# Kernel optimization log

Hardware: AMD Instinct MI355X
Metric: run time of the kernel (lower is better)

## Reference

```python
import jax, jax.numpy as jnp
import numpy as np

L, C, H = 4, 512, 8
HD = C // H

def silu(x):
    return x * jax.nn.sigmoid(x)

def layernorm(x, g, b, eps=1e-5):
    m = x.mean(-1, keepdims=True)
    v = ((x - m) ** 2).mean(-1, keepdims=True)
    return (x - m) * jax.lax.rsqrt(v + eps) * g + b

def adaln(x, t, w, b):
    # x: (N,B,C), t: (B,C), w: (2C,C), b: (2C,)
    mod = silu(t) @ w.T + b
    scale, shift = jnp.split(mod, 2, axis=-1)
    return x * (1.0 + scale[None]) + shift[None]

def embed_rotary(x, pos):
    # x: (B,N,C), pos: (B,N,C,2) with [...,0]=cos, [...,1]=sin
    cos, sin = pos[..., 0], pos[..., 1]
    x2 = jnp.stack([-x[..., 1::2], x[..., 0::2]], axis=-1).reshape(x.shape)
    return x * cos + x2 * sin

def setup_inputs() -> dict:
    key = jax.random.key(0)
    ks = jax.random.split(key, 24)
    Nq, Nkv, B = 1024, 2048, 4
    query = jax.random.normal(ks[0], (Nq, B, C), jnp.float32)
    value = jax.random.normal(ks[1], (Nkv, B, C), jnp.float32)
    diff_ts = jax.random.normal(ks[2], (B, C), jnp.float32)
    # valid rotary codes: cos/sin of random angles
    aq = jax.random.uniform(ks[3], (B, Nq, C), jnp.float32, 0.0, 2 * np.pi)
    ak = jax.random.uniform(ks[4], (B, Nkv, C), jnp.float32, 0.0, 2 * np.pi)
    query_pos = jnp.stack([jnp.cos(aq), jnp.sin(aq)], axis=-1)
    value_pos = jnp.stack([jnp.cos(ak), jnp.sin(ak)], axis=-1)
    s = 0.02
    inp = dict(query=query, value=value, diff_ts=diff_ts,
               query_pos=query_pos, value_pos=value_pos,
               aw_attn=jax.random.normal(ks[5], (L, 2 * C, C)) * s,
               ab_attn=jax.random.normal(ks[6], (L, 2 * C)) * s,
               in_w=jax.random.normal(ks[7], (L, 3 * C, C)) * s,
               in_b=jnp.zeros((L, 3 * C)),
               out_w=jax.random.normal(ks[8], (L, C, C)) * s,
               out_b=jnp.zeros((L, C)),
               ln1_g=jnp.ones((L, C)), ln1_b=jnp.zeros((L, C)),
               aw_ffn=jax.random.normal(ks[9], (L, 2 * C, C)) * s,
               ab_ffn=jax.random.normal(ks[10], (L, 2 * C)) * s,
               w1=jax.random.normal(ks[11], (L, C, C)) * s,
               b1=jnp.zeros((L, C)),
               w2=jax.random.normal(ks[12], (L, C, C)) * s,
               b2=jnp.zeros((L, C)),
               ln2_g=jnp.ones((L, C)), ln2_b=jnp.zeros((L, C)))
    return inp

def _forward(query, value, diff_ts, query_pos, value_pos,
             aw_attn, ab_attn, in_w, in_b, out_w, out_b, ln1_g, ln1_b,
             aw_ffn, ab_ffn, w1, b1, w2, b2, ln2_g, ln2_b):
    Nq, B, _ = query.shape
    Nkv = value.shape[0]
    scaling = HD ** -0.5
    outputs = []
    q = query
    for i in range(L):
        # --- cross-attention layer ---
        aq = adaln(q, diff_ts, aw_attn[i], ab_attn[i])
        wq, wk, wv = jnp.split(in_w[i], 3, axis=0)
        bq, bk, bv = jnp.split(in_b[i], 3, axis=0)
        qp = (aq @ wq.T + bq) * scaling          # (Nq,B,C)
        kp = value @ wk.T + bk                    # (Nkv,B,C)
        vp = value @ wv.T + bv
        qb = embed_rotary(qp.transpose(1, 0, 2), query_pos)  # (B,Nq,C)
        kb = embed_rotary(kp.transpose(1, 0, 2), value_pos)  # (B,Nkv,C)
        vb = vp.transpose(1, 0, 2)
        qh = qb.reshape(B, Nq, H, HD).transpose(0, 2, 1, 3)   # (B,H,Nq,HD)
        kh = kb.reshape(B, Nkv, H, HD).transpose(0, 2, 1, 3)
        vh = vb.reshape(B, Nkv, H, HD).transpose(0, 2, 1, 3)
        scores = jnp.einsum('bhqd,bhkd->bhqk', qh, kh)
        attn = jax.nn.softmax(scores, axis=-1)
        o = jnp.einsum('bhqk,bhkd->bhqd', attn, vh)
        o = o.transpose(0, 2, 1, 3).reshape(B, Nq, C).transpose(1, 0, 2)  # (Nq,B,C)
        o = o @ out_w[i].T + out_b[i]
        q = layernorm(q + o, ln1_g[i], ln1_b[i])
        # --- feedforward layer (residual uses AdaLN-modulated x) ---
        xa = adaln(q, diff_ts, aw_ffn[i], ab_ffn[i])
        h = jax.nn.relu(xa @ w1[i].T + b1[i])
        h = h @ w2[i].T + b2[i]
        q = layernorm(xa + h, ln2_g[i], ln2_b[i])
        outputs.append(q)
    return jnp.stack(outputs)  # (L, Nq, B, C)

def reference(query, value, diff_ts, query_pos, value_pos,
              aw_attn, ab_attn, in_w, in_b, out_w, out_b, ln1_g, ln1_b,
              aw_ffn, ab_ffn, w1, b1, w2, b2, ln2_g, ln2_b):
    return _forward(query, value, diff_ts, query_pos, value_pos,
                    aw_attn, ab_attn, in_w, in_b, out_w, out_b, ln1_g, ln1_b,
                    aw_ffn, ab_ffn, w1, b1, w2, b2, ln2_g, ln2_b)
```

## Files before the change

### kernel.cpp

```cpp
#include <hip/hip_runtime.h>
#include <hip/hip_bf16.h>

typedef __hip_bfloat16 bf16;
typedef __attribute__((ext_vector_type(8))) short short8;
typedef __attribute__((ext_vector_type(4))) float f32x4;

#define CDIM 512
#define BDIM 4
#define HDIM 8
#define HDQ  64
#define NQ   1024
#define NKV  2048
#define LAYERS 4
#define SPLIT 2

#if defined(__has_builtin)
#if __has_builtin(__builtin_amdgcn_global_load_lds)
#define USE_GLL 1
#endif
#endif

static __device__ __forceinline__ short f2s(float f) {
    bf16 h = __float2bfloat16(f);
    return *reinterpret_cast<short*>(&h);
}


__global__ __launch_bounds__(256) void conv_f2b(const float* __restrict__ in,
                                                bf16* __restrict__ out, int n) {
    int i = blockIdx.x * 256 + threadIdx.x;
    if (i < n) out[i] = __float2bfloat16(in[i]);
}

__global__ __launch_bounds__(256) void silu_k(const float* __restrict__ t,
                                              float* __restrict__ st) {
    int i = blockIdx.x * 256 + threadIdx.x;
    float x = t[i];
    st[i] = x / (1.f + __expf(-x));
}

__global__ __launch_bounds__(256) void modall_k(const float* __restrict__ st,
    const float* __restrict__ aw_attn, const float* __restrict__ ab_attn,
    const float* __restrict__ aw_ffn,  const float* __restrict__ ab_ffn,
    float* __restrict__ mod) {
    int wv = blockIdx.x * 4 + (threadIdx.x >> 6);
    int lane = threadIdx.x & 63;
    int col  = wv & 1023;
    int b    = (wv >> 10) & 3;
    int kind = (wv >> 12) & 1;
    int l    = wv >> 13;
    const float* w = (kind ? aw_ffn : aw_attn) + ((size_t)l * 1024 + col) * CDIM + lane * 8;
    const float* tb = st + b * CDIM + lane * 8;
    f32x4 w0 = *(const f32x4*)w;
    f32x4 w1 = *(const f32x4*)(w + 4);
    f32x4 t0 = *(const f32x4*)tb;
    f32x4 t1 = *(const f32x4*)(tb + 4);
    f32x4 pp = w0 * t0 + w1 * t1;
    float acc = (pp[0] + pp[1]) + (pp[2] + pp[3]);
    #pragma unroll
    for (int off = 32; off; off >>= 1) acc += __shfl_xor(acc, off);
    if (lane == 0)
        mod[wv] = acc + (kind ? ab_ffn : ab_attn)[l * 1024 + col];
}

__global__ __launch_bounds__(256) void adaln_k(const float* __restrict__ x,
                                               const float* __restrict__ mod,
                                               bf16* __restrict__ outb) {
    int i = blockIdx.x * 256 + threadIdx.x;
    int c = i & 511;
    int b = (i >> 9) & 3;
    outb[i] = __float2bfloat16(x[i] * (1.f + mod[b * 1024 + c]) + mod[b * 1024 + 512 + c]);
}

__global__ __launch_bounds__(256) void ln_ad_k(const float* __restrict__ x,
                                               const float* __restrict__ res,
                                               const float* __restrict__ g,
                                               const float* __restrict__ bb,
                                               const float* __restrict__ mod,
                                               float* __restrict__ ln_f,
                                               float* __restrict__ ln_f2,
                                               float* __restrict__ ad_f,
                                               bf16* __restrict__ ad_b) {
    int row = blockIdx.x;
    int t = threadIdx.x;
    size_t base = (size_t)row * CDIM;
    float v0 = x[base + t] + res[base + t];
    float v1 = x[base + t + 256] + res[base + t + 256];
    float s1 = v0 + v1;
    float s2 = v0 * v0 + v1 * v1;
    #pragma unroll
    for (int off = 32; off; off >>= 1) {
        s1 += __shfl_xor(s1, off);
        s2 += __shfl_xor(s2, off);
    }
    __shared__ float a1[4], a2[4];
    int w = t >> 6;
    if ((t & 63) == 0) { a1[w] = s1; a2[w] = s2; }
    __syncthreads();
    s1 = a1[0] + a1[1] + a1[2] + a1[3];
    s2 = a2[0] + a2[1] + a2[2] + a2[3];
    float mean = s1 * (1.f / 512.f);
    float var = s2 * (1.f / 512.f) - mean * mean;
    float rs = rsqrtf(var + 1e-5f);
    float y0 = (v0 - mean) * rs * g[t] + bb[t];
    float y1 = (v1 - mean) * rs * g[t + 256] + bb[t + 256];
    if (ln_f)  { ln_f[base + t] = y0;  ln_f[base + t + 256] = y1; }
    if (ln_f2) { ln_f2[base + t] = y0; ln_f2[base + t + 256] = y1; }
    if (mod) {
        int b = row & 3;
        float o0 = y0 * (1.f + mod[b * 1024 + t]) + mod[b * 1024 + 512 + t];
        float o1 = y1 * (1.f + mod[b * 1024 + t + 256]) + mod[b * 1024 + 512 + t + 256];
        if (ad_f) { ad_f[base + t] = o0; ad_f[base + t + 256] = o1; }
        ad_b[base + t] = __float2bfloat16(o0);
        ad_b[base + t + 256] = __float2bfloat16(o1);
    }
}

template <int EPI, int WM, int NT>
__global__ __launch_bounds__(256) void mgemm_k(
    const bf16* __restrict__ A, const bf16* __restrict__ Wt,
    const float* __restrict__ bias, void* __restrict__ out0v,
    void* __restrict__ out1v, int M, int N, int K,
    const float* __restrict__ pos, float scl, int Nseq) {
    __shared__ bf16 As[2][WM * 32 * 32];
    __shared__ bf16 Bs[2][NT * 32 * 32];
    const int BM = WM * 32;
    const int BN = NT * 32;
    int t = threadIdx.x;
    int w = t >> 6;
    int lane = t & 63;
    int l16 = lane & 15;
    int quad = lane >> 4;
    int wy = w >> 1, wx = w & 1;
    int bm = blockIdx.y * BM;
    int bn = blockIdx.x * BN;
#if USE_GLL
    int lr = lane >> 2;
    int lq = lane & 3;
#endif

    f32x4 acc[WM][NT] = {};

    auto stage = [&](int buf, int k0) {
#if USE_GLL
        if (w < 2) {
            const bf16* src = A + (size_t)(bm + w * (WM * 16)) * K + k0;
            bf16* dstb = As[buf] + (w * (WM * 16)) * 32;
            #pragma unroll
            for (int i = 0; i < WM; ++i) {
                __builtin_amdgcn_global_load_lds(
                    (const unsigned int __attribute__((address_space(1)))*)
                        (src + ((size_t)(i * 16 + lr)) * K + lq * 8),
                    (unsigned int __attribute__((address_space(3)))*)
                        (dstb + i * 16 * 32),
                    16, 0, 0);
            }
        } else {
            const bf16* src = Wt + (size_t)(bn + (w - 2) * (NT * 16)) * K + k0;
            bf16* dstb = Bs[buf] + ((w - 2) * (NT * 16)) * 32;
            #pragma unroll
            for (int i = 0; i < NT; ++i) {
                __builtin_amdgcn_global_load_lds(
                    (const unsigned int __attribute__((address_space(1)))*)
                        (src + ((size_t)(i * 16 + lr)) * K + lq * 8),
                    (unsigned int __attribute__((address_space(3)))*)
                        (dstb + i * 16 * 32),
                    16, 0, 0);
            }
        }
#else
        for (int e = t; e < BM * 4; e += 256) {
            int row = e >> 2, kq = e & 3;
            *(uint4*)&As[buf][row * 32 + kq * 8] =
                *(const uint4*)(A + (size_t)(bm + row) * K + k0 + kq * 8);
        }
        for (int e = t; e < BN * 4; e += 256) {
            int row = e >> 2, kq = e & 3;
            *(uint4*)&Bs[buf][row * 32 + kq * 8] =
                *(const uint4*)(Wt + (size_t)(bn + row) * K + k0 + kq * 8);
        }
#endif
    };

    stage(0, 0);
    __syncthreads();
    int cur = 0;

    for (int k0 = 0; k0 < K; k0 += 32) {
        if (k0 + 32 < K) stage(cur ^ 1, k0 + 32);

        short8 af[WM], bfr[NT];
        #pragma unroll
        for (int mt = 0; mt < WM; ++mt)
            af[mt] = *(const short8*)&As[cur][((wy * WM + mt) * 16 + l16) * 32 + quad * 8];
        #pragma unroll
        for (int nt = 0; nt < NT; ++nt)
            bfr[nt] = *(const short8*)&Bs[cur][((wx * NT + nt) * 16 + l16) * 32 + quad * 8];
        #pragma unroll
        for (int mt = 0; mt < WM; ++mt)
            #pragma unroll
            for (int nt = 0; nt < NT; ++nt)
                acc[mt][nt] = __builtin_amdgcn_mfma_f32_16x16x32_bf16(
                    af[mt], bfr[nt], acc[mt][nt], 0, 0, 0);

        __syncthreads();
        cur ^= 1;
    }

    #pragma unroll
    for (int nt = 0; nt < NT; ++nt) {
        int n = bn + (wx * NT + nt) * 16 + l16;
        float bnv = (EPI == 4) ? 0.f : bias[n];
        #pragma unroll
        for (int mt = 0; mt < WM; ++mt) {
            #pragma unroll
            for (int r = 0; r < 4; ++r) {
                int m = bm + (wy * WM + mt) * 16 + quad * 4 + r;
                float v = acc[mt][nt][r] + ((EPI == 4) ? bias[m] : bnv);
                if (EPI == 0) {
                    ((float*)out0v)[(size_t)m * N + n] = v;
                } else if (EPI == 1) {
                    ((bf16*)out0v)[(size_t)m * N + n] = __float2bfloat16(fmaxf(v, 0.f));
                } else if (EPI == 4) {
                    int hh = m >> 6, dd = m & 63;
                    int bsel = n & 3, key = n >> 2;
                    ((bf16*)out0v)[((size_t)(bsel * HDIM + hh) * HDQ + dd) * NKV + key] =
                        __float2bfloat16(v);
                } else {
                    v *= scl;
                    int c = n;
                    int nseq = m >> 2, b = m & 3;
                    float part = __shfl_xor(v, 1);
                    const float* pp = pos + (((size_t)b * Nseq + nseq) * CDIM + c) * 2;
                    float cs = pp[0], sn = pp[1];
                    float o = (l16 & 1) ? (v * cs + part * sn) : (v * cs - part * sn);
                    bf16* op = (bf16*)out0v +
                               ((size_t)(b * HDIM + (c >> 6)) * Nseq + nseq) * HDQ + (c & 63);
                    *op = __float2bfloat16(o);
                }
            }
        }
    }
}

__global__ __launch_bounds__(256) void attn4_k(const bf16* __restrict__ qh,
                                               const bf16* __restrict__ kh,
                                               const bf16* __restrict__ vT,
                                               float* __restrict__ pl,
                                               float* __restrict__ pacc) {
    __shared__ short Kb[2][64 * 64];
    __shared__ short Vb[2][64 * 64];
    __shared__ short Ps[4][16 * 64];
    int t = threadIdx.x;
    int wave = t >> 6, lane = t & 63;
    int l16 = lane & 15, quad = lane >> 4;
    int bh = blockIdx.y;
    int q0 = blockIdx.x * 64 + wave * 16;
    int kbase = blockIdx.z * (NKV / SPLIT);

    const bf16* qbase = qh + ((size_t)bh * NQ + q0) * HDQ;
    short8 aq0 = *(const short8*)(qbase + (size_t)l16 * HDQ + quad * 8);
    short8 aq1 = *(const short8*)(qbase + (size_t)l16 * HDQ + 32 + quad * 8);
    const bf16* kbh = kh + ((size_t)bh * NKV + kbase) * HDQ;
    const bf16* vbh = vT + (size_t)bh * HDQ * NKV + kbase;

    int r0 = wave * 16;
    int lr = lane >> 3;
    int swz_src = ((lane & 7) ^ lr) * 8;

    auto stage = [&](int buf, int kt) {
#if USE_GLL
        #pragma unroll
        for (int j = 0; j < 2; ++j) {
            int rr = r0 + j * 8;
            __builtin_amdgcn_global_load_lds(
                (const unsigned int __attribute__((address_space(1)))*)
                    (kbh + (size_t)(kt + rr + lr) * HDQ + swz_src),
                (unsigned int __attribute__((address_space(3)))*)&Kb[buf][rr * 64],
                16, 0, 0);
            __builtin_amdgcn_global_load_lds(
                (const unsigned int __attribute__((address_space(1)))*)
                    (vbh + (size_t)(rr + lr) * NKV + kt + swz_src),
                (unsigned int __attribute__((address_space(3)))*)&Vb[buf][rr * 64],
                16, 0, 0);
        }
#else
        #pragma unroll
        for (int j = 0; j < 2; ++j) {
            int rr = r0 + j * 8 + lr;
            int lc = lane & 7;
            *(short8*)&Kb[buf][rr * 64 + ((lc ^ (rr & 7)) * 8)] =
                *(const short8*)(kbh + (size_t)(kt + rr) * HDQ + lc * 8);
            *(short8*)&Vb[buf][rr * 64 + ((lc ^ (rr & 7)) * 8)] =
                *(const short8*)(vbh + (size_t)rr * NKV + kt + lc * 8);
        }
#endif
    };

    f32x4 accO[4] = {};
    float lsum[4] = {0.f, 0.f, 0.f, 0.f};

    stage(0, 0);
    __syncthreads();
    int cur = 0;
    int swz_m = l16 & 7;

    for (int kt = 0; kt < NKV / SPLIT; kt += 64) {
        if (kt + 64 < NKV / SPLIT) stage(cur ^ 1, kt + 64);

        f32x4 sc[4] = {};
        #pragma unroll
        for (int nt = 0; nt < 4; ++nt) {
            const short* kr = &Kb[cur][(nt * 16 + l16) * 64];
            short8 bk0 = *(const short8*)&kr[(quad ^ swz_m) * 8];
            short8 bk1 = *(const short8*)&kr[((quad + 4) ^ swz_m) * 8];
            sc[nt] = __builtin_amdgcn_mfma_f32_16x16x32_bf16(aq0, bk0, sc[nt], 0, 0, 0);
            sc[nt] = __builtin_amdgcn_mfma_f32_16x16x32_bf16(aq1, bk1, sc[nt], 0, 0, 0);
        }

        #pragma unroll
        for (int r = 0; r < 4; ++r) {
            float p0 = exp2f(sc[0][r]);
            float p1 = exp2f(sc[1][r]);
            float p2 = exp2f(sc[2][r]);
            float p3 = exp2f(sc[3][r]);
            lsum[r] += (p0 + p1) + (p2 + p3);
            int pr = quad * 4 + r;
            short* prow = &Ps[wave][pr * 64];
            int pm = pr & 7;
            int ch = l16 >> 3, kl = l16 & 7;
            prow[((ch ^ pm) << 3) + kl]       = f2s(p0);
            prow[(((ch + 2) ^ pm) << 3) + kl] = f2s(p1);
            prow[(((ch + 4) ^ pm) << 3) + kl] = f2s(p2);
            prow[(((ch + 6) ^ pm) << 3) + kl] = f2s(p3);
        }

        const short* prd = &Ps[wave][l16 * 64];
        short8 pa0 = *(const short8*)&prd[(quad ^ swz_m) * 8];
        short8 pa1 = *(const short8*)&prd[((quad + 4) ^ swz_m) * 8];
        #pragma unroll
        for (int nt = 0; nt < 4; ++nt) {
            const short* vr = &Vb[cur][(nt * 16 + l16) * 64];
            short8 bv0 = *(const short8*)&vr[(quad ^ swz_m) * 8];
            short8 bv1 = *(const short8*)&vr[((quad + 4) ^ swz_m) * 8];
            accO[nt] = __builtin_amdgcn_mfma_f32_16x16x32_bf16(pa0, bv0, accO[nt], 0, 0, 0);
            accO[nt] = __builtin_amdgcn_mfma_f32_16x16x32_bf16(pa1, bv1, accO[nt], 0, 0, 0);
        }

        __syncthreads();
        cur ^= 1;
    }

    #pragma unroll
    for (int r = 0; r < 4; ++r) {
        #pragma unroll
        for (int off = 1; off < 16; off <<= 1) lsum[r] += __shfl_xor(lsum[r], off);
    }

    size_t rowbase = ((size_t)blockIdx.z * 32 + bh) * NQ + q0;
    #pragma unroll
    for (int r = 0; r < 4; ++r) {
        size_t row = rowbase + quad * 4 + r;
        if (l16 == 0) pl[row] = lsum[r];
        #pragma unroll
        for (int nt = 0; nt < 4; ++nt)
            pacc[row * 64 + nt * 16 + l16] = accO[nt][r];
    }
}

__global__ __launch_bounds__(256) void attn_comb_k(const float* __restrict__ pl,
                                                   const float* __restrict__ pacc,
                                                   bf16* __restrict__ o) {
    int idx = blockIdx.x * 256 + threadIdx.x;
    int d = idx & 63;
    int row = idx >> 6;
    int q = row & (NQ - 1);
    int bh = row >> 10;
    const int S = 32 * NQ;
    float l = pl[row] + pl[S + row];
    float v = pacc[(size_t)row * 64 + d] + pacc[(size_t)(S + row) * 64 + d];
    int b = bh >> 3, h = bh & 7;
    o[((size_t)(q * BDIM + b)) * CDIM + h * HDQ + d] = __float2bfloat16(v / l);
}


extern "C" void kernel_launch(void* const* d_in, const int* in_sizes, int n_in,
                              void* d_out, int out_size, void* d_ws, size_t ws_size,
                              hipStream_t stream) {
    const float* query     = (const float*)d_in[0];
    const float* value     = (const float*)d_in[1];
    const float* diff_ts   = (const float*)d_in[2];
    const float* query_pos = (const float*)d_in[3];
    const float* value_pos = (const float*)d_in[4];
    const float* aw_attn   = (const float*)d_in[5];
    const float* ab_attn   = (const float*)d_in[6];
    const float* in_w      = (const float*)d_in[7];
    const float* in_b      = (const float*)d_in[8];
    const float* out_w     = (const float*)d_in[9];
    const float* out_b     = (const float*)d_in[10];
    const float* ln1_g     = (const float*)d_in[11];
    const float* ln1_b     = (const float*)d_in[12];
    const float* aw_ffn    = (const float*)d_in[13];
    const float* ab_ffn    = (const float*)d_in[14];
    const float* w1        = (const float*)d_in[15];
    const float* b1        = (const float*)d_in[16];
    const float* w2        = (const float*)d_in[17];
    const float* b2        = (const float*)d_in[18];
    const float* ln2_g     = (const float*)d_in[19];
    const float* ln2_b     = (const float*)d_in[20];
    float* out_f = (float*)d_out;

    float* ws      = (float*)d_ws;
    float* st      = ws;
    float* mod_ws  = ws + 2048;
    float* q_cur   = ws + 34816;
    float* buf_a   = q_cur + 2097152;
    float* buf_p   = buf_a + 2097152;
    bf16* a_bf     = (bf16*)(buf_p + 2097152);
    bf16* h_bf     = a_bf + 2097152;
    bf16* qh       = h_bf + 2097152;
    bf16* kh       = qh + 2097152;
    bf16* vt       = kh + 4194304;
    bf16* val_bf   = vt + 4194304;
    bf16* winb     = val_bf + 4194304;
    bf16* woutb    = winb + 3145728;
    bf16* w1b      = woutb + 1048576;
    bf16* w2b      = w1b + 1048576;
    float* pacc    = buf_a;
    float* pl      = (float*)a_bf;

    const int MQ = NQ * BDIM;
    const int MKV = NKV * BDIM;
    const float scaling = 0.125f * 1.44269504f;

    silu_k<<<8, 256, 0, stream>>>(diff_ts, st);
    modall_k<<<8192, 256, 0, stream>>>(st, aw_attn, ab_attn, aw_ffn, ab_ffn, mod_ws);
    conv_f2b<<<16384, 256, 0, stream>>>(value, val_bf, 4194304);
    conv_f2b<<<12288, 256, 0, stream>>>(in_w, winb, 3145728);
    conv_f2b<<<4096, 256, 0, stream>>>(out_w, woutb, 1048576);
    conv_f2b<<<4096, 256, 0, stream>>>(w1, w1b, 1048576);
    conv_f2b<<<4096, 256, 0, stream>>>(w2, w2b, 1048576);
    adaln_k<<<(MQ * CDIM) / 256, 256, 0, stream>>>(query, mod_ws, a_bf);

    for (int i = 0; i < LAYERS; ++i) {
        const float* mod_ffn  = mod_ws + i * 8192 + 4096;
        const float* mod_attn_next = (i + 1 < LAYERS) ? (mod_ws + (i + 1) * 8192) : nullptr;
        const bf16* winb_i = winb + (size_t)i * 1536 * CDIM;
        const float* in_b_i = in_b + (size_t)i * 1536;
        const float* qsrc = (i == 0) ? query : q_cur;

        mgemm_k<2, 2, 2><<<dim3(8, MQ / 64), 256, 0, stream>>>(
            a_bf, winb_i, in_b_i, qh, nullptr, MQ, 512, CDIM, query_pos, scaling, NQ);
        mgemm_k<2, 2, 2><<<dim3(8, MKV / 64), 256, 0, stream>>>(
            val_bf, winb_i + (size_t)512 * CDIM, in_b_i + 512, kh, nullptr, MKV, 512,
            CDIM, value_pos, 1.f, NKV);
        mgemm_k<4, 2, 2><<<dim3(MKV / 64, 8), 256, 0, stream>>>(
            winb_i + (size_t)1024 * CDIM, val_bf, in_b_i + 1024, vt, nullptr,
            512, MKV, CDIM, nullptr, 0.f, 0);
        attn4_k<<<dim3(NQ / 64, BDIM * HDIM, SPLIT), 256, 0, stream>>>(
            qh, kh, vt, pl, pacc);
        attn_comb_k<<<8192, 256, 0, stream>>>(pl, pacc, h_bf);
        mgemm_k<0, 2, 2><<<dim3(8, MQ / 64), 256, 0, stream>>>(
            h_bf, woutb + (size_t)i * CDIM * CDIM, out_b + i * CDIM, buf_p, nullptr,
            MQ, 512, CDIM, nullptr, 0.f, 0);
        ln_ad_k<<<MQ, 256, 0, stream>>>(qsrc, buf_p, ln1_g + i * CDIM, ln1_b + i * CDIM,
                                        mod_ffn, nullptr, nullptr, buf_a, a_bf);
        mgemm_k<1, 2, 2><<<dim3(8, MQ / 64), 256, 0, stream>>>(
            a_bf, w1b + (size_t)i * CDIM * CDIM, b1 + i * CDIM, h_bf, nullptr,
            MQ, 512, CDIM, nullptr, 0.f, 0);
        mgemm_k<0, 2, 2><<<dim3(8, MQ / 64), 256, 0, stream>>>(
            h_bf, w2b + (size_t)i * CDIM * CDIM, b2 + i * CDIM, buf_p, nullptr,
            MQ, 512, CDIM, nullptr, 0.f, 0);
        ln_ad_k<<<MQ, 256, 0, stream>>>(buf_a, buf_p, ln2_g + i * CDIM, ln2_b + i * CDIM,
                                        mod_attn_next, q_cur,
                                        out_f + (size_t)i * MQ * CDIM, nullptr, a_bf);
    }
}
```

Before: 729.7 us.

## Fuse conversion kernels, fold SiLU into modulation, deepen GEMM K-step to 64

Measured after the change: 701.5 us. 3.9% less time.

```diff
diff --git a/kernel.cpp b/kernel.cpp
--- a/kernel.cpp
+++ b/kernel.cpp
@@ -3,6 +3,7 @@
 
 typedef __hip_bfloat16 bf16;
 typedef __attribute__((ext_vector_type(8))) short short8;
+typedef __attribute__((ext_vector_type(4))) short s16x4;
 typedef __attribute__((ext_vector_type(4))) float f32x4;
 
 #define CDIM 512
@@ -26,20 +27,26 @@
 }
 
 
-__global__ __launch_bounds__(256) void conv_f2b(const float* __restrict__ in,
-                                                bf16* __restrict__ out, int n) {
-    int i = blockIdx.x * 256 + threadIdx.x;
-    if (i < n) out[i] = __float2bfloat16(in[i]);
-}
-
-__global__ __launch_bounds__(256) void silu_k(const float* __restrict__ t,
-                                              float* __restrict__ st) {
-    int i = blockIdx.x * 256 + threadIdx.x;
-    float x = t[i];
-    st[i] = x / (1.f + __expf(-x));
-}
-
-__global__ __launch_bounds__(256) void modall_k(const float* __restrict__ st,
+__global__ __launch_bounds__(256) void convall_k(
+    const float* __restrict__ s0, const float* __restrict__ s1,
+    const float* __restrict__ s2, const float* __restrict__ s3,
+    const float* __restrict__ s4,
+    bf16* __restrict__ d0, bf16* __restrict__ d1, bf16* __restrict__ d2,
+    bf16* __restrict__ d3, bf16* __restrict__ d4) {
+    int gid = blockIdx.x * 256 + threadIdx.x;
+    const float* src; bf16* dst; int off;
+    if (gid < 1048576)      { src = s0; dst = d0; off = gid; }
+    else if (gid < 1835008) { src = s1; dst = d1; off = gid - 1048576; }
+    else if (gid < 2097152) { src = s2; dst = d2; off = gid - 1835008; }
+    else if (gid < 2359296) { src = s3; dst = d3; off = gid - 2097152; }
+    else                    { src = s4; dst = d4; off = gid - 2359296; }
+    f32x4 v = *(const f32x4*)(src + (size_t)off * 4);
+    s16x4 o;
+    o[0] = f2s(v[0]); o[1] = f2s(v[1]); o[2] = f2s(v[2]); o[3] = f2s(v[3]);
+    *(s16x4*)(dst + (size_t)off * 4) = o;
+}
+
+__global__ __launch_bounds__(256) void modall_k(const float* __restrict__ diff_ts,
     const float* __restrict__ aw_attn, const float* __restrict__ ab_attn,
     const float* __restrict__ aw_ffn,  const float* __restrict__ ab_ffn,
     float* __restrict__ mod) {
@@ -50,11 +57,16 @@
     int kind = (wv >> 12) & 1;
     int l    = wv >> 13;
     const float* w = (kind ? aw_ffn : aw_attn) + ((size_t)l * 1024 + col) * CDIM + lane * 8;
-    const float* tb = st + b * CDIM + lane * 8;
+    const float* tb = diff_ts + b * CDIM + lane * 8;
     f32x4 w0 = *(const f32x4*)w;
     f32x4 w1 = *(const f32x4*)(w + 4);
     f32x4 t0 = *(const f32x4*)tb;
     f32x4 t1 = *(const f32x4*)(tb + 4);
+    #pragma unroll
+    for (int j = 0; j < 4; ++j) {
+        t0[j] = t0[j] / (1.f + __expf(-t0[j]));
+        t1[j] = t1[j] / (1.f + __expf(-t1[j]));
+    }
     f32x4 pp = w0 * t0 + w1 * t1;
     float acc = (pp[0] + pp[1]) + (pp[2] + pp[3]);
     #pragma unroll
@@ -122,62 +134,44 @@
     const float* __restrict__ bias, void* __restrict__ out0v,
     void* __restrict__ out1v, int M, int N, int K,
     const float* __restrict__ pos, float scl, int Nseq) {
-    __shared__ bf16 As[2][WM * 32 * 32];
-    __shared__ bf16 Bs[2][NT * 32 * 32];
-    const int BM = WM * 32;
-    const int BN = NT * 32;
+    __shared__ bf16 As[2][2][64 * 32];
+    __shared__ bf16 Bs[2][2][64 * 32];
     int t = threadIdx.x;
     int w = t >> 6;
     int lane = t & 63;
     int l16 = lane & 15;
     int quad = lane >> 4;
     int wy = w >> 1, wx = w & 1;
-    int bm = blockIdx.y * BM;
-    int bn = blockIdx.x * BN;
-#if USE_GLL
-    int lr = lane >> 2;
-    int lq = lane & 3;
-#endif
+    int bm = blockIdx.y * 64;
+    int bn = blockIdx.x * 64;
+    int lr2 = lane >> 2;
+    int lc4 = lane & 3;
 
     f32x4 acc[WM][NT] = {};
 
     auto stage = [&](int buf, int k0) {
 #if USE_GLL
-        if (w < 2) {
-            const bf16* src = A + (size_t)(bm + w * (WM * 16)) * K + k0;
-            bf16* dstb = As[buf] + (w * (WM * 16)) * 32;
-            #pragma unroll
-            for (int i = 0; i < WM; ++i) {
-                __builtin_amdgcn_global_load_lds(
-                    (const unsigned int __attribute__((address_space(1)))*)
-                        (src + ((size_t)(i * 16 + lr)) * K + lq * 8),
-                    (unsigned int __attribute__((address_space(3)))*)
-                        (dstb + i * 16 * 32),
-                    16, 0, 0);
-            }
-        } else {
-            const bf16* src = Wt + (size_t)(bn + (w - 2) * (NT * 16)) * K + k0;
-            bf16* dstb = Bs[buf] + ((w - 2) * (NT * 16)) * 32;
-            #pragma unroll
-            for (int i = 0; i < NT; ++i) {
-                __builtin_amdgcn_global_load_lds(
-                    (const unsigned int __attribute__((address_space(1)))*)
-                        (src + ((size_t)(i * 16 + lr)) * K + lq * 8),
-                    (unsigned int __attribute__((address_space(3)))*)
-                        (dstb + i * 16 * 32),
-                    16, 0, 0);
-            }
+        const bf16* sa = A + (size_t)(bm + w * 16 + lr2) * K + k0 + lc4 * 8;
+        const bf16* sb = Wt + (size_t)(bn + w * 16 + lr2) * K + k0 + lc4 * 8;
+        #pragma unroll
+        for (int j = 0; j < 2; ++j) {
+            __builtin_amdgcn_global_load_lds(
+                (const unsigned int __attribute__((address_space(1)))*)(sa + j * 32),
+                (unsigned int __attribute__((address_space(3)))*)(&As[buf][j][w * 512]),
+                16, 0, 0);
+            __builtin_amdgcn_global_load_lds(
+                (const unsigned int __attribute__((address_space(1)))*)(sb + j * 32),
+                (unsigned int __attribute__((address_space(3)))*)(&Bs[buf][j][w * 512]),
+                16, 0, 0);
         }
 #else
-        for (int e = t; e < BM * 4; e += 256) {
-            int row = e >> 2, kq = e & 3;
-            *(uint4*)&As[buf][row * 32 + kq * 8] =
-                *(const uint4*)(A + (size_t)(bm + row) * K + k0 + kq * 8);
-        }
-        for (int e = t; e < BN * 4; e += 256) {
-            int row = e >> 2, kq = e & 3;
-            *(uint4*)&Bs[buf][row * 32 + kq * 8] =
-                *(const uint4*)(Wt + (size_t)(bn + row) * K + k0 + kq * 8);
+        for (int e = t; e < 512; e += 256) {
+            int sub = e >> 8, c = e & 255;
+            int row = c >> 2, c4 = c & 3;
+            *(uint4*)&As[buf][sub][row * 32 + c4 * 8] =
+                *(const uint4*)(A + (size_t)(bm + row) * K + k0 + sub * 32 + c4 * 8);
+            *(uint4*)&Bs[buf][sub][row * 32 + c4 * 8] =
+                *(const uint4*)(Wt + (size_t)(bn + row) * K + k0 + sub * 32 + c4 * 8);
         }
 #endif
     };
@@ -186,22 +180,27 @@
     __syncthreads();
     int cur = 0;
 
-    for (int k0 = 0; k0 < K; k0 += 32) {
-        if (k0 + 32 < K) stage(cur ^ 1, k0 + 32);
-
-        short8 af[WM], bfr[NT];
-        #pragma unroll
-        for (int mt = 0; mt < WM; ++mt)
-            af[mt] = *(const short8*)&As[cur][((wy * WM + mt) * 16 + l16) * 32 + quad * 8];
-        #pragma unroll
-        for (int nt = 0; nt < NT; ++nt)
-            bfr[nt] = *(const short8*)&Bs[cur][((wx * NT + nt) * 16 + l16) * 32 + quad * 8];
-        #pragma unroll
-        for (int mt = 0; mt < WM; ++mt)
+    for (int k0 = 0; k0 < K; k0 += 64) {
+        if (k0 + 64 < K) stage(cur ^ 1, k0 + 64);
+
+        #pragma unroll
+        for (int kk = 0; kk < 2; ++kk) {
+            short8 af[WM], bfr[NT];
+            #pragma unroll
+            for (int mt = 0; mt < WM; ++mt)
+                af[mt] = *(const short8*)
+                    &As[cur][kk][((wy * WM + mt) * 16 + l16) * 32 + quad * 8];
             #pragma unroll
             for (int nt = 0; nt < NT; ++nt)
-                acc[mt][nt] = __builtin_amdgcn_mfma_f32_16x16x32_bf16(
-                    af[mt], bfr[nt], acc[mt][nt], 0, 0, 0);
+                bfr[nt] = *(const short8*)
+                    &Bs[cur][kk][((wx * NT + nt) * 16 + l16) * 32 + quad * 8];
+            #pragma unroll
+            for (int mt = 0; mt < WM; ++mt)
+                #pragma unroll
+                for (int nt = 0; nt < NT; ++nt)
+                    acc[mt][nt] = __builtin_amdgcn_mfma_f32_16x16x32_bf16(
+                        af[mt], bfr[nt], acc[mt][nt], 0, 0, 0);
+        }
 
         __syncthreads();
         cur ^= 1;
@@ -411,7 +410,6 @@
     float* out_f = (float*)d_out;
 
     float* ws      = (float*)d_ws;
-    float* st      = ws;
     float* mod_ws  = ws + 2048;
     float* q_cur   = ws + 34816;
     float* buf_a   = q_cur + 2097152;
@@ -433,13 +431,9 @@
     const int MKV = NKV * BDIM;
     const float scaling = 0.125f * 1.44269504f;
 
-    silu_k<<<8, 256, 0, stream>>>(diff_ts, st);
-    modall_k<<<8192, 256, 0, stream>>>(st, aw_attn, ab_attn, aw_ffn, ab_ffn, mod_ws);
-    conv_f2b<<<16384, 256, 0, stream>>>(value, val_bf, 4194304);
-    conv_f2b<<<12288, 256, 0, stream>>>(in_w, winb, 3145728);
-    conv_f2b<<<4096, 256, 0, stream>>>(out_w, woutb, 1048576);
-    conv_f2b<<<4096, 256, 0, stream>>>(w1, w1b, 1048576);
-    conv_f2b<<<4096, 256, 0, stream>>>(w2, w2b, 1048576);
+    modall_k<<<8192, 256, 0, stream>>>(diff_ts, aw_attn, ab_attn, aw_ffn, ab_ffn, mod_ws);
+    convall_k<<<10240, 256, 0, stream>>>(value, in_w, out_w, w1, w2,
+                                         val_bf, winb, woutb, w1b, w2b);
     adaln_k<<<(MQ * CDIM) / 256, 256, 0, stream>>>(query, mod_ws, a_bf);
 
     for (int i = 0; i < LAYERS; ++i) {
```
